# Kernel optimization log

Measured on AMD Instinct MI355X. Metric: run time of the kernel, lower is better.

Reference implementation:

```python
import jax, jax.numpy as jnp
import numpy as np

NUM_EXPERTS = 8
CAPACITY_C = 1.0
ROUTER_TEMP = 1.0
EPS = 1e-10


def reference(x, router_w, router_b, w_gate, b_gate, w_up, b_up, w_down, b_down):
    # x: [B, S, H]
    B, S, H = x.shape
    n_tok = B * S
    k = int(n_tok * CAPACITY_C) // NUM_EXPERTS  # expert capacity (1024 here)

    xf = x.reshape(n_tok, H)  # (b s) h

    # Linear router (dropout p=0 -> identity), computed in float32 as in .float()
    clean_h = xf @ router_w + router_b  # [n_tok, E]

    # Gumbel noise (deterministic key stands in for torch.rand_like)
    u = jax.random.uniform(jax.random.key(42), clean_h.shape, dtype=clean_h.dtype)
    gumbel = -jnp.log(-jnp.log(u + EPS) + EPS)
    h = (clean_h + gumbel) / ROUTER_TEMP

    Sm = jax.nn.softmax(h, axis=-1)  # softmax over experts

    # top-k over the TOKEN dim (dim=0) per expert -> expert-choice routing
    Gt, idxt = jax.lax.top_k(Sm.T, k)  # [E, k]
    G = Gt.T            # [k, E] routing weights
    idx = idxt.T        # [k, E] chosen token indices

    # Gather routed tokens (replaces the one-hot einsum gather exactly:
    # top-k indices are distinct per expert, so one-hot matmul == take)
    toks = jnp.take(xf, idx, axis=0)  # [k, E, H]

    # Shared SwiGLU FFN (group_size=1 -> one expert instance reused E times)
    gate = jax.nn.silu(toks @ w_gate + b_gate)  # [k, E, dff]
    up = toks @ w_up + b_up                      # [k, E, dff]
    e_out = (gate * up) @ w_down + b_down        # [k, E, H]

    # Weight by G and scatter-add back to token positions, summed over experts
    weighted = G[..., None] * e_out              # [k, E, H]
    y = jnp.zeros_like(xf).at[idx.reshape(-1)].add(weighted.reshape(-1, H))
    return y.reshape(B, S, H)


def setup_inputs() -> dict:
    key = jax.random.key(0)
    ks = jax.random.split(key, 6)
    B, S, H, E = 4, 2048, 2048, NUM_EXPERTS
    dff = int(H * 4 * 2 / 3)  # 5461
    sH = 1.0 / np.sqrt(H)
    sF = 1.0 / np.sqrt(dff)
    return {
        "x": jax.random.normal(ks[0], (B, S, H), dtype=jnp.float32),
        "router_w": jax.random.normal(ks[1], (H, E), dtype=jnp.float32) * sH,
        "router_b": jnp.zeros((E,), dtype=jnp.float32),
        "w_gate": jax.random.normal(ks[2], (H, dff), dtype=jnp.float32) * sH,
        "b_gate": jnp.zeros((dff,), dtype=jnp.float32),
        "w_up": jax.random.normal(ks[3], (H, dff), dtype=jnp.float32) * sH,
        "b_up": jnp.zeros((dff,), dtype=jnp.float32),
        "w_down": jax.random.normal(ks[4], (dff, H), dtype=jnp.float32) * sF,
        "b_down": jnp.zeros((H,), dtype=jnp.float32),
    }
```

## Files before the change

### kernel.cpp

```cpp
#include <hip/hip_runtime.h>
#include <cstdint>
#include <cstddef>

#define N_TOK  8192
#define HDIM   2048
#define NEXP   8
#define KCAP   1024
#define DFF    5461
#define DFF_PB 5504
#define ACT_P  5504
#define NT1    (HDIM / 64)
#define NT2    (ACT_P / 64)

typedef unsigned short u16;
typedef short bf16x8 __attribute__((ext_vector_type(8)));
typedef float f32x4  __attribute__((ext_vector_type(4)));

__device__ __forceinline__ u16 f2bf(float f) {
  uint32_t u = __float_as_uint(f);
  uint32_t r = (u + 0x7FFFu + ((u >> 16) & 1u)) >> 16;
  return (u16)r;
}

__device__ __forceinline__ uint32_t rotl32(uint32_t v, int d) {
  return (v << d) | (v >> (32 - d));
}

__device__ uint32_t threefry_bits(uint32_t idx) {
  const uint32_t ks0 = 0u, ks1 = 42u, ks2 = 0u ^ 42u ^ 0x1BD11BDAu;
  uint32_t x0 = 0u + ks0;
  uint32_t x1 = idx + ks1;
#define TFR(d) { x0 += x1; x1 = rotl32(x1, d); x1 ^= x0; }
  TFR(13) TFR(15) TFR(26) TFR(6)
  x0 += ks1; x1 += ks2 + 1u;
  TFR(17) TFR(29) TFR(16) TFR(24)
  x0 += ks2; x1 += ks0 + 2u;
  TFR(13) TFR(15) TFR(26) TFR(6)
  x0 += ks0; x1 += ks1 + 3u;
  TFR(17) TFR(29) TFR(16) TFR(24)
  x0 += ks1; x1 += ks2 + 4u;
  TFR(13) TFR(15) TFR(26) TFR(6)
  x0 += ks2; x1 += ks0 + 5u;
#undef TFR
  return x0 ^ x1;
}

__global__ __launch_bounds__(256) void router_kernel(const float* __restrict__ x,
    const float* __restrict__ rw, const float* __restrict__ rb,
    float* __restrict__ SmT)
{
  const int lane = threadIdx.x & 63;
  const int wid  = threadIdx.x >> 6;
  const int t = blockIdx.x * 4 + wid;
  const float* xr = x + (size_t)t * HDIM;
  float acc[8] = {0.f,0.f,0.f,0.f,0.f,0.f,0.f,0.f};
#pragma unroll
  for (int it = 0; it < HDIM / 64; ++it) {
    int h = lane + it * 64;
    float xv = xr[h];
    const float4* wp = (const float4*)(rw + h * 8);
    float4 w0 = wp[0], w1 = wp[1];
    acc[0] = fmaf(xv, w0.x, acc[0]);
    acc[1] = fmaf(xv, w0.y, acc[1]);
    acc[2] = fmaf(xv, w0.z, acc[2]);
    acc[3] = fmaf(xv, w0.w, acc[3]);
    acc[4] = fmaf(xv, w1.x, acc[4]);
    acc[5] = fmaf(xv, w1.y, acc[5]);
    acc[6] = fmaf(xv, w1.z, acc[6]);
    acc[7] = fmaf(xv, w1.w, acc[7]);
  }
#pragma unroll
  for (int m = 32; m >= 1; m >>= 1) {
#pragma unroll
    for (int e = 0; e < 8; ++e) acc[e] += __shfl_xor(acc[e], m, 64);
  }
  if (lane == 0) {
    float h[8];
#pragma unroll
    for (int e = 0; e < 8; ++e) {
      uint32_t bits = threefry_bits((uint32_t)(t * 8 + e));
      float u = __uint_as_float((bits >> 9) | 0x3f800000u) - 1.0f;
      u = fmaxf(u, 0.0f);
      float g = -logf(-logf(u + 1e-10f) + 1e-10f);
      h[e] = acc[e] + rb[e] + g;
    }
    float mx = h[0];
#pragma unroll
    for (int e = 1; e < 8; ++e) mx = fmaxf(mx, h[e]);
    float ex[8]; float s = 0.f;
#pragma unroll
    for (int e = 0; e < 8; ++e) { ex[e] = expf(h[e] - mx); s += ex[e]; }
#pragma unroll
    for (int e = 0; e < 8; ++e) SmT[e * N_TOK + t] = ex[e] / s;
  }
}

__global__ __launch_bounds__(1024) void select_topk(const float* __restrict__ SmT,
    uint32_t* __restrict__ selTok, float* __restrict__ selW)
{
  const int e = blockIdx.x;
  const int tid = threadIdx.x;
  const float* v = SmT + (size_t)e * N_TOK;
  __shared__ uint32_t hist[256];
  __shared__ uint32_t sh_byte, sh_kk, sh_cnt, sh_eqc;
  uint32_t bitsv[8];
#pragma unroll
  for (int i = 0; i < 8; ++i) bitsv[i] = __float_as_uint(v[tid + i * 1024]);
  uint32_t prefix = 0;
  uint32_t kk = KCAP;
  for (int s = 3; s >= 0; --s) {
    if (tid < 256) hist[tid] = 0;
    __syncthreads();
    uint32_t himask = (s == 3) ? 0u : (0xFFFFFFFFu << ((s + 1) * 8));
#pragma unroll
    for (int i = 0; i < 8; ++i) {
      uint32_t b = bitsv[i];
      if ((b & himask) == prefix) atomicAdd(&hist[(b >> (s * 8)) & 255u], 1u);
    }
    __syncthreads();
    if (tid == 0) {
      uint32_t cum = 0; uint32_t bsel = 0, kn = kk;
      for (int b = 255; b >= 0; --b) {
        uint32_t c = hist[b];
        if (cum + c >= kk) { bsel = (uint32_t)b; kn = kk - cum; break; }
        cum += c;
      }
      sh_byte = bsel; sh_kk = kn;
    }
    __syncthreads();
    prefix |= sh_byte << (s * 8);
    kk = sh_kk;
  }
  const uint32_t T = prefix;
  const uint32_t need = kk;
  if (tid == 0) { sh_cnt = 0; sh_eqc = 0; }
  __syncthreads();
#pragma unroll
  for (int i = 0; i < 8; ++i) {
    uint32_t b = bitsv[i];
    if (b > T) {
      uint32_t p = atomicAdd(&sh_cnt, 1u);
      selTok[e * KCAP + p] = (uint32_t)(tid + i * 1024);
      selW[e * KCAP + p] = __uint_as_float(b);
    } else if (b == T) {
      atomicAdd(&sh_eqc, 1u);
    }
  }
  __syncthreads();
  if (sh_eqc == need) {
#pragma unroll
    for (int i = 0; i < 8; ++i) {
      if (bitsv[i] == T) {
        uint32_t p = atomicAdd(&sh_cnt, 1u);
        selTok[e * KCAP + p] = (uint32_t)(tid + i * 1024);
        selW[e * KCAP + p] = __uint_as_float(T);
      }
    }
  } else if (tid == 0) {
    uint32_t p = sh_cnt, rem = need;
    for (int t = 0; t < N_TOK && rem > 0u; ++t) {
      if (__float_as_uint(v[t]) == T) {
        selTok[e * KCAP + p] = (uint32_t)t;
        selW[e * KCAP + p] = __uint_as_float(T);
        ++p; --rem;
      }
    }
  }
}

__global__ __launch_bounds__(256) void build_inv(const uint32_t* __restrict__ selTok,
    int* __restrict__ inv)
{
  int s = blockIdx.x * 256 + threadIdx.x;
  inv[(s >> 10) * N_TOK + (int)selTok[s]] = s;
}

__global__ __launch_bounds__(256) void gather_kernel(const float* __restrict__ x,
    const uint32_t* __restrict__ selTok, u16* __restrict__ Xsel)
{
  const int slot = blockIdx.x;
  const int tid = threadIdx.x;
  const uint32_t tok = selTok[slot];
  const float4* src = (const float4*)(x + (size_t)tok * HDIM);
  float4 a = src[tid * 2], b = src[tid * 2 + 1];
  union { u16 h[8]; uint4 vv; } pk;
  pk.h[0] = f2bf(a.x); pk.h[1] = f2bf(a.y); pk.h[2] = f2bf(a.z); pk.h[3] = f2bf(a.w);
  pk.h[4] = f2bf(b.x); pk.h[5] = f2bf(b.y); pk.h[6] = f2bf(b.z); pk.h[7] = f2bf(b.w);
  ((uint4*)(Xsel + (size_t)slot * HDIM))[tid] = pk.vv;
}

__global__ __launch_bounds__(256) void transpose_convert(const float* __restrict__ in,
    int rows_in, int cols_in, u16* __restrict__ out, int out_cols)
{
  __shared__ float tile[32][33];
  const int bi = blockIdx.y;
  const int bj = blockIdx.x;
  const int tx = threadIdx.x, ty = threadIdx.y;
#pragma unroll
  for (int t = 0; t < 4; ++t) {
    int r = bi * 32 + ty + t * 8, c = bj * 32 + tx;
    float vv = (r < rows_in && c < cols_in) ? in[(size_t)r * cols_in + c] : 0.0f;
    tile[ty + t * 8][tx] = vv;
  }
  __syncthreads();
#pragma unroll
  for (int t = 0; t < 4; ++t) {
    int oj = bj * 32 + ty + t * 8;
    int oi = bi * 32 + tx;
    out[(size_t)oj * out_cols + oi] = f2bf(tile[tx][ty + t * 8]);
  }
}

#if defined(__has_builtin)
#  if __has_builtin(__builtin_amdgcn_global_load_lds)
#    define HAVE_GLD 1
#  endif
#endif
#ifdef HAVE_GLD
#define STG(gp, lp) __builtin_amdgcn_global_load_lds( \
    (const __attribute__((address_space(1))) void*)(gp), \
    (__attribute__((address_space(3))) void*)(lp), 16, 0, 0)
#define WAITV4() asm volatile("s_waitcnt vmcnt(4)" ::: "memory")
#define WAITV2() asm volatile("s_waitcnt vmcnt(2)" ::: "memory")
#define WAITV0() asm volatile("s_waitcnt vmcnt(0)" ::: "memory")
#else
#define STG(gp, lp) (*(bf16x8*)(lp) = *(const bf16x8*)(gp))
#define WAITV4() asm volatile("s_waitcnt vmcnt(0) lgkmcnt(0)" ::: "memory")
#define WAITV2() asm volatile("s_waitcnt vmcnt(0) lgkmcnt(0)" ::: "memory")
#define WAITV0() asm volatile("s_waitcnt vmcnt(0) lgkmcnt(0)" ::: "memory")
#endif
#define BAR()    __builtin_amdgcn_s_barrier()
#define SCHED0() __builtin_amdgcn_sched_barrier(0)
#define PRIO1()  __builtin_amdgcn_s_setprio(1)
#define PRIO0()  __builtin_amdgcn_s_setprio(0)
#define MFMA(a, b, c) __builtin_amdgcn_mfma_f32_16x16x32_bf16(a, b, c, 0, 0, 0)


__global__ __launch_bounds__(512, 2) void gemm1_kernel(
    const u16* __restrict__ Xsel,
    const u16* __restrict__ WgT,
    const u16* __restrict__ WuT,
    const float* __restrict__ bg, const float* __restrict__ bu,
    u16* __restrict__ act)
{
  __shared__ u16 AL[2][2][8192];
  __shared__ u16 GL[2][8192];
  __shared__ u16 UL[2][8192];

  const int id = blockIdx.x;
  const int wg = (id & 7) * 172 + (id >> 3);
  const int bm = wg & 31;
  const int bn = wg >> 5;

  const int tid = threadIdx.x;
  const int lane = tid & 63, wid = tid >> 6;
  const int wm = wid >> 2, wn = wid & 3;
  const int fr = lane & 15, ck = lane >> 4;
  const int sw0 = (ck ^ (fr & 7)) * 8;
  const int sw1 = sw0 ^ 32;
  const int rA = (wm * 64 + fr) * 64;
  const int rB = (wn * 32 + fr) * 64;

  const int sr = tid >> 3;
  const int sq = (tid & 7) ^ (sr & 7);
  const u16* aS0 = Xsel + (size_t)(bm * 256 + sr) * HDIM + sq * 8;
  const u16* aS1 = aS0 + (size_t)128 * HDIM;
  const u16* gS  = WgT + (size_t)(bn * 128 + sr) * HDIM + sq * 8;
  const u16* uS  = WuT + (size_t)(bn * 128 + sr) * HDIM + sq * 8;

#define ST_A0(kt) { u16* d = &AL[(kt)&1][0][tid*8]; \
    STG(aS0 + (kt)*64, d); STG(aS0 + (kt)*64 + (size_t)64*HDIM, d + 4096); }
#define ST_A1(kt) { u16* d = &AL[(kt)&1][1][tid*8]; \
    STG(aS1 + (kt)*64, d); STG(aS1 + (kt)*64 + (size_t)64*HDIM, d + 4096); }
#define ST_G(kt) { u16* d = &GL[(kt)&1][tid*8]; \
    STG(gS + (kt)*64, d); STG(gS + (kt)*64 + (size_t)64*HDIM, d + 4096); }
#define ST_U(kt) { u16* d = &UL[(kt)&1][tid*8]; \
    STG(uS + (kt)*64, d); STG(uS + (kt)*64 + (size_t)64*HDIM, d + 4096); }

  f32x4 accg[8][2], accu[8][2];
  const f32x4 z4 = {0.f, 0.f, 0.f, 0.f};
#pragma unroll
  for (int i = 0; i < 8; ++i)
#pragma unroll
    for (int n = 0; n < 2; ++n) { accg[i][n] = z4; accu[i][n] = z4; }

  bf16x8 af[4][2], bgf[2][2], buf[2][2];

  ST_A0(0) ST_G(0) ST_U(0) ST_A1(0)
  WAITV4(); BAR();

  for (int kt = 0; kt < NT1; ++kt) {
    const u16* A0 = AL[kt & 1][0];
    const u16* A1 = AL[kt & 1][1];
    const u16* G  = GL[kt & 1];
    const u16* U  = UL[kt & 1];
    const int st = (kt + 1 < NT1);
#pragma unroll
    for (int i = 0; i < 4; ++i) {
      af[i][0] = *(const bf16x8*)&A0[rA + i * 1024 + sw0];
      af[i][1] = *(const bf16x8*)&A0[rA + i * 1024 + sw1];
    }
#pragma unroll
    for (int n = 0; n < 2; ++n) {
      bgf[n][0] = *(const bf16x8*)&G[rB + n * 1024 + sw0];
      bgf[n][1] = *(const bf16x8*)&G[rB + n * 1024 + sw1];
    }
    if (st) ST_A0(kt + 1)
    BAR(); SCHED0();
    PRIO1();
#pragma unroll
    for (int ks = 0; ks < 2; ++ks)
#pragma unroll
      for (int i = 0; i < 4; ++i)
#pragma unroll
        for (int n = 0; n < 2; ++n)
          accg[i][n] = MFMA(af[i][ks], bgf[n][ks], accg[i][n]);
    PRIO0();
    if (st) { WAITV4(); } else { WAITV2(); }
    BAR();
#pragma unroll
    for (int n = 0; n < 2; ++n) {
      buf[n][0] = *(const bf16x8*)&U[rB + n * 1024 + sw0];
      buf[n][1] = *(const bf16x8*)&U[rB + n * 1024 + sw1];
    }
    if (st) ST_G(kt + 1)
    BAR(); SCHED0();
    PRIO1();
#pragma unroll
    for (int ks = 0; ks < 2; ++ks)
#pragma unroll
      for (int i = 0; i < 4; ++i)
#pragma unroll
        for (int n = 0; n < 2; ++n)
          accu[i][n] = MFMA(af[i][ks], buf[n][ks], accu[i][n]);
    PRIO0();
    if (st) { WAITV4(); } else { WAITV0(); }
    BAR();
#pragma unroll
    for (int i = 0; i < 4; ++i) {
      af[i][0] = *(const bf16x8*)&A1[rA + i * 1024 + sw0];
      af[i][1] = *(const bf16x8*)&A1[rA + i * 1024 + sw1];
    }
    if (st) ST_U(kt + 1)
    BAR(); SCHED0();
    PRIO1();
#pragma unroll
    for (int ks = 0; ks < 2; ++ks)
#pragma unroll
      for (int i = 0; i < 4; ++i)
#pragma unroll
        for (int n = 0; n < 2; ++n)
          accg[4 + i][n] = MFMA(af[i][ks], bgf[n][ks], accg[4 + i][n]);
    PRIO0();
    if (st) ST_A1(kt + 1)
    PRIO1();
#pragma unroll
    for (int ks = 0; ks < 2; ++ks)
#pragma unroll
      for (int i = 0; i < 4; ++i)
#pragma unroll
        for (int n = 0; n < 2; ++n)
          accu[4 + i][n] = MFMA(af[i][ks], buf[n][ks], accu[4 + i][n]);
    PRIO0();
    WAITV4();
    BAR();
  }

#pragma unroll
  for (int f = 0; f < 8; ++f) {
    const int rbase = bm * 256 + (f >> 2) * 128 + wm * 64 + (f & 3) * 16 + ck * 4;
#pragma unroll
    for (int v = 0; v < 4; ++v) {
      u16* arow = act + (size_t)(rbase + v) * ACT_P;
#pragma unroll
      for (int n = 0; n < 2; ++n) {
        const int col = bn * 128 + wn * 32 + n * 16 + fr;
        u16 ov = 0;
        if (col < DFF) {
          float gv = accg[f][n][v] + bg[col];
          float uv = accu[f][n][v] + bu[col];
          ov = f2bf((gv / (1.0f + expf(-gv))) * uv);
        }
        arow[col] = ov;
      }
    }
  }
#undef ST_A0
#undef ST_A1
#undef ST_G
#undef ST_U
}

__global__ __launch_bounds__(512, 2) void gemm2_kernel(
    const u16* __restrict__ act,
    const u16* __restrict__ WdT,
    const float* __restrict__ bd,
    const float* __restrict__ selW,
    float* __restrict__ Yslot)
{
  __shared__ u16 AL[2][2][8192];
  __shared__ u16 BL[2][2][8192];

  const int id = blockIdx.x;
  const int wg = (id & 7) * 32 + (id >> 3);
  const int bm = wg & 31, bn = wg >> 5;

  const int tid = threadIdx.x;
  const int lane = tid & 63, wid = tid >> 6;
  const int wm = wid >> 2, wn = wid & 3;
  const int fr = lane & 15, ck = lane >> 4;
  const int sw0 = (ck ^ (fr & 7)) * 8;
  const int sw1 = sw0 ^ 32;
  const int rA = (wm * 64 + fr) * 64;
  const int rB = (wn * 32 + fr) * 64;

  const int sr = tid >> 3;
  const int sq = (tid & 7) ^ (sr & 7);
  const u16* aS0 = act + (size_t)(bm * 256 + sr) * ACT_P + sq * 8;
  const u16* aS1 = aS0 + (size_t)128 * ACT_P;
  const u16* bS0 = WdT + (size_t)(bn * 256 + sr) * ACT_P + sq * 8;
  const u16* bS1 = bS0 + (size_t)128 * ACT_P;

#define ST_A0(kt) { u16* d = &AL[(kt)&1][0][tid*8]; \
    STG(aS0 + (kt)*64, d); STG(aS0 + (kt)*64 + (size_t)64*ACT_P, d + 4096); }
#define ST_A1(kt) { u16* d = &AL[(kt)&1][1][tid*8]; \
    STG(aS1 + (kt)*64, d); STG(aS1 + (kt)*64 + (size_t)64*ACT_P, d + 4096); }
#define ST_B0(kt) { u16* d = &BL[(kt)&1][0][tid*8]; \
    STG(bS0 + (kt)*64, d); STG(bS0 + (kt)*64 + (size_t)64*ACT_P, d + 4096); }
#define ST_B1(kt) { u16* d = &BL[(kt)&1][1][tid*8]; \
    STG(bS1 + (kt)*64, d); STG(bS1 + (kt)*64 + (size_t)64*ACT_P, d + 4096); }

  f32x4 acc[8][4];
  const f32x4 z4 = {0.f, 0.f, 0.f, 0.f};
#pragma unroll
  for (int i = 0; i < 8; ++i)
#pragma unroll
    for (int n = 0; n < 4; ++n) acc[i][n] = z4;

  bf16x8 af[4][2], b0[2][2], b1[2][2];

  ST_A0(0) ST_B0(0) ST_B1(0) ST_A1(0)
  WAITV4(); BAR();

  for (int kt = 0; kt < NT2; ++kt) {
    const u16* A0 = AL[kt & 1][0];
    const u16* A1 = AL[kt & 1][1];
    const u16* B0 = BL[kt & 1][0];
    const u16* B1 = BL[kt & 1][1];
    const int st = (kt + 1 < NT2);
#pragma unroll
    for (int i = 0; i < 4; ++i) {
      af[i][0] = *(const bf16x8*)&A0[rA + i * 1024 + sw0];
      af[i][1] = *(const bf16x8*)&A0[rA + i * 1024 + sw1];
    }
#pragma unroll
    for (int n = 0; n < 2; ++n) {
      b0[n][0] = *(const bf16x8*)&B0[rB + n * 1024 + sw0];
      b0[n][1] = *(const bf16x8*)&B0[rB + n * 1024 + sw1];
    }
    if (st) ST_A0(kt + 1)
    BAR(); SCHED0();
    PRIO1();
#pragma unroll
    for (int ks = 0; ks < 2; ++ks)
#pragma unroll
      for (int i = 0; i < 4; ++i)
#pragma unroll
        for (int n = 0; n < 2; ++n)
          acc[i][n] = MFMA(af[i][ks], b0[n][ks], acc[i][n]);
    PRIO0();
    if (st) { WAITV4(); } else { WAITV2(); }
    BAR();
#pragma unroll
    for (int n = 0; n < 2; ++n) {
      b1[n][0] = *(const bf16x8*)&B1[rB + n * 1024 + sw0];
      b1[n][1] = *(const bf16x8*)&B1[rB + n * 1024 + sw1];
    }
    if (st) ST_B0(kt + 1)
    BAR(); SCHED0();
    PRIO1();
#pragma unroll
    for (int ks = 0; ks < 2; ++ks)
#pragma unroll
      for (int i = 0; i < 4; ++i)
#pragma unroll
        for (int n = 0; n < 2; ++n)
          acc[i][2 + n] = MFMA(af[i][ks], b1[n][ks], acc[i][2 + n]);
    PRIO0();
    if (st) { WAITV4(); } else { WAITV0(); }
    BAR();
#pragma unroll
    for (int i = 0; i < 4; ++i) {
      af[i][0] = *(const bf16x8*)&A1[rA + i * 1024 + sw0];
      af[i][1] = *(const bf16x8*)&A1[rA + i * 1024 + sw1];
    }
    if (st) ST_B1(kt + 1)
    BAR(); SCHED0();
    PRIO1();
#pragma unroll
    for (int ks = 0; ks < 2; ++ks)
#pragma unroll
      for (int i = 0; i < 4; ++i)
#pragma unroll
        for (int n = 0; n < 2; ++n)
          acc[4 + i][n] = MFMA(af[i][ks], b0[n][ks], acc[4 + i][n]);
    PRIO0();
    if (st) ST_A1(kt + 1)
    PRIO1();
#pragma unroll
    for (int ks = 0; ks < 2; ++ks)
#pragma unroll
      for (int i = 0; i < 4; ++i)
#pragma unroll
        for (int n = 0; n < 2; ++n)
          acc[4 + i][2 + n] = MFMA(af[i][ks], b1[n][ks], acc[4 + i][2 + n]);
    PRIO0();
    WAITV4();
    BAR();
  }

#pragma unroll
  for (int f = 0; f < 8; ++f) {
    const int rbase = bm * 256 + (f >> 2) * 128 + wm * 64 + (f & 3) * 16 + ck * 4;
#pragma unroll
    for (int v = 0; v < 4; ++v) {
      const int srow = rbase + v;
      const float w = selW[srow];
      float* yrow = Yslot + (size_t)srow * HDIM;
#pragma unroll
      for (int n = 0; n < 4; ++n) {
        const int col = bn * 256 + (n >> 1) * 128 + wn * 32 + (n & 1) * 16 + fr;
        yrow[col] = w * (acc[f][n][v] + bd[col]);
      }
    }
  }
#undef ST_A0
#undef ST_A1
#undef ST_B0
#undef ST_B1
}

__global__ __launch_bounds__(256) void scatter_kernel(const float* __restrict__ Yslot,
    const int* __restrict__ inv, float* __restrict__ y)
{
  const int t = blockIdx.x;
  const int c = threadIdx.x * 8;
  float4 a0 = {0.f,0.f,0.f,0.f}, a1 = {0.f,0.f,0.f,0.f};
#pragma unroll
  for (int e = 0; e < 8; ++e) {
    const int s = inv[e * N_TOK + t];
    if (s >= 0) {
      const float4* p = (const float4*)(Yslot + (size_t)s * HDIM + c);
      float4 v0 = p[0], v1 = p[1];
      a0.x += v0.x; a0.y += v0.y; a0.z += v0.z; a0.w += v0.w;
      a1.x += v1.x; a1.y += v1.y; a1.z += v1.z; a1.w += v1.w;
    }
  }
  float4* yp = (float4*)(y + (size_t)t * HDIM + c);
  yp[0] = a0; yp[1] = a1;
}

extern "C" void kernel_launch(void* const* d_in, const int* in_sizes, int n_in,
                              void* d_out, int out_size, void* d_ws, size_t ws_size,
                              hipStream_t stream) {
  const float* x      = (const float*)d_in[0];
  const float* rw     = (const float*)d_in[1];
  const float* rb     = (const float*)d_in[2];
  const float* w_gate = (const float*)d_in[3];
  const float* b_gate = (const float*)d_in[4];
  const float* w_up   = (const float*)d_in[5];
  const float* b_up   = (const float*)d_in[6];
  const float* w_down = (const float*)d_in[7];
  const float* b_down = (const float*)d_in[8];
  float* y = (float*)d_out;

  uint8_t* ws = (uint8_t*)d_ws;
  uint32_t* selTok = (uint32_t*)(ws + 0);
  float*    selW   = (float*)(ws + 32768);
  int*      inv    = (int*)(ws + 65536);
  u16*      act    = (u16*)(ws + 327680);
  u16*      Xsel   = (u16*)(ws + 90505216ull);
  u16*      WdT    = (u16*)(ws + 90505216ull);
  float*    Yslot  = (float*)(ws + 113049600ull);
  float*    SmT    = (float*)(ws + 124059648ull);
  u16*      WgT    = (u16*)(ws + 124321792ull);
  u16*      WuT    = (u16*)(ws + 146866176ull);

  hipMemsetAsync(inv, 0xFF, NEXP * N_TOK * sizeof(int), stream);
  transpose_convert<<<dim3(172, 64), dim3(32, 8), 0, stream>>>(w_gate, 2048, DFF, WgT, 2048);
  transpose_convert<<<dim3(172, 64), dim3(32, 8), 0, stream>>>(w_up,   2048, DFF, WuT, 2048);
  router_kernel<<<N_TOK / 4, 256, 0, stream>>>(x, rw, rb, SmT);
  select_topk<<<NEXP, 1024, 0, stream>>>(SmT, selTok, selW);
  build_inv<<<N_TOK / 256, 256, 0, stream>>>(selTok, inv);
  gather_kernel<<<N_TOK, 256, 0, stream>>>(x, selTok, Xsel);
  gemm1_kernel<<<43 * 32, 512, 0, stream>>>(Xsel, WgT, WuT, b_gate, b_up, act);
  transpose_convert<<<dim3(64, 172), dim3(32, 8), 0, stream>>>(w_down, DFF, 2048, WdT, ACT_P);
  gemm2_kernel<<<8 * 32, 512, 0, stream>>>(act, WdT, b_down, selW, Yslot);
  scatter_kernel<<<N_TOK, 256, 0, stream>>>(Yslot, inv, y);
}
```

Before: 911.0 us.

## Trim GEMM pipeline barriers, batch B-tile prefetches, remap gemm1 blocks per XCD

Both GEMM kernels drop the barrier that separated the LDS fragment reads from the next-tile global-to-LDS prefetch. The two B-operand prefetches are now issued together, with a matching vmcnt(6) wait. The second-half gate/up (or b0/b1) MFMA loops are merged into one interleaved loop, and sched barriers now follow the remaining barriers. gemm1 also maps blocks so that each XCD owns four consecutive row tiles, which should improve L2 reuse of the A operand. The SiLU epilogue switches to __expf and a hardware reciprocal. The gains target fewer barrier stalls and longer MFMA runs, at the cost of tighter reliance on correct waitcnt accounting and slightly less precise SiLU.

```diff
diff --git a/kernel.cpp b/kernel.cpp
--- a/kernel.cpp
+++ b/kernel.cpp
@@ -220,11 +220,13 @@
 #define STG(gp, lp) __builtin_amdgcn_global_load_lds( \
     (const __attribute__((address_space(1))) void*)(gp), \
     (__attribute__((address_space(3))) void*)(lp), 16, 0, 0)
+#define WAITV6() asm volatile("s_waitcnt vmcnt(6)" ::: "memory")
 #define WAITV4() asm volatile("s_waitcnt vmcnt(4)" ::: "memory")
 #define WAITV2() asm volatile("s_waitcnt vmcnt(2)" ::: "memory")
 #define WAITV0() asm volatile("s_waitcnt vmcnt(0)" ::: "memory")
 #else
 #define STG(gp, lp) (*(bf16x8*)(lp) = *(const bf16x8*)(gp))
+#define WAITV6() asm volatile("s_waitcnt vmcnt(0) lgkmcnt(0)" ::: "memory")
 #define WAITV4() asm volatile("s_waitcnt vmcnt(0) lgkmcnt(0)" ::: "memory")
 #define WAITV2() asm volatile("s_waitcnt vmcnt(0) lgkmcnt(0)" ::: "memory")
 #define WAITV0() asm volatile("s_waitcnt vmcnt(0) lgkmcnt(0)" ::: "memory")
@@ -248,9 +250,10 @@
   __shared__ u16 UL[2][8192];
 
   const int id = blockIdx.x;
-  const int wg = (id & 7) * 172 + (id >> 3);
-  const int bm = wg & 31;
-  const int bn = wg >> 5;
+  const int xcd = id & 7;
+  const int r = id >> 3;
+  const int bm = xcd * 4 + (r & 3);
+  const int bn = r >> 2;
 
   const int tid = threadIdx.x;
   const int lane = tid & 63, wid = tid >> 6;
@@ -287,7 +290,7 @@
   bf16x8 af[4][2], bgf[2][2], buf[2][2];
 
   ST_A0(0) ST_G(0) ST_U(0) ST_A1(0)
-  WAITV4(); BAR();
+  WAITV4(); BAR(); SCHED0();
 
   for (int kt = 0; kt < NT1; ++kt) {
     const u16* A0 = AL[kt & 1][0];
@@ -306,7 +309,6 @@
       bgf[n][1] = *(const bf16x8*)&G[rB + n * 1024 + sw1];
     }
     if (st) ST_A0(kt + 1)
-    BAR(); SCHED0();
     PRIO1();
 #pragma unroll
     for (int ks = 0; ks < 2; ++ks)
@@ -317,14 +319,13 @@
           accg[i][n] = MFMA(af[i][ks], bgf[n][ks], accg[i][n]);
     PRIO0();
     if (st) { WAITV4(); } else { WAITV2(); }
-    BAR();
+    BAR(); SCHED0();
 #pragma unroll
     for (int n = 0; n < 2; ++n) {
       buf[n][0] = *(const bf16x8*)&U[rB + n * 1024 + sw0];
       buf[n][1] = *(const bf16x8*)&U[rB + n * 1024 + sw1];
     }
-    if (st) ST_G(kt + 1)
-    BAR(); SCHED0();
+    if (st) { ST_G(kt + 1) ST_U(kt + 1) }
     PRIO1();
 #pragma unroll
     for (int ks = 0; ks < 2; ++ks)
@@ -334,24 +335,13 @@
         for (int n = 0; n < 2; ++n)
           accu[i][n] = MFMA(af[i][ks], buf[n][ks], accu[i][n]);
     PRIO0();
-    if (st) { WAITV4(); } else { WAITV0(); }
-    BAR();
+    if (st) { WAITV6(); } else { WAITV0(); }
+    BAR(); SCHED0();
 #pragma unroll
     for (int i = 0; i < 4; ++i) {
       af[i][0] = *(const bf16x8*)&A1[rA + i * 1024 + sw0];
       af[i][1] = *(const bf16x8*)&A1[rA + i * 1024 + sw1];
     }
-    if (st) ST_U(kt + 1)
-    BAR(); SCHED0();
-    PRIO1();
-#pragma unroll
-    for (int ks = 0; ks < 2; ++ks)
-#pragma unroll
-      for (int i = 0; i < 4; ++i)
-#pragma unroll
-        for (int n = 0; n < 2; ++n)
-          accg[4 + i][n] = MFMA(af[i][ks], bgf[n][ks], accg[4 + i][n]);
-    PRIO0();
     if (st) ST_A1(kt + 1)
     PRIO1();
 #pragma unroll
@@ -359,11 +349,13 @@
 #pragma unroll
       for (int i = 0; i < 4; ++i)
 #pragma unroll
-        for (int n = 0; n < 2; ++n)
+        for (int n = 0; n < 2; ++n) {
+          accg[4 + i][n] = MFMA(af[i][ks], bgf[n][ks], accg[4 + i][n]);
           accu[4 + i][n] = MFMA(af[i][ks], buf[n][ks], accu[4 + i][n]);
+        }
     PRIO0();
     WAITV4();
-    BAR();
+    BAR(); SCHED0();
   }
 
 #pragma unroll
@@ -379,7 +371,9 @@
         if (col < DFF) {
           float gv = accg[f][n][v] + bg[col];
           float uv = accu[f][n][v] + bu[col];
-          ov = f2bf((gv / (1.0f + expf(-gv))) * uv);
+          float e = __expf(-gv);
+          float sv = gv * __builtin_amdgcn_rcpf(1.0f + e);
+          ov = f2bf(sv * uv);
         }
         arow[col] = ov;
       }
@@ -440,7 +434,7 @@
   bf16x8 af[4][2], b0[2][2], b1[2][2];
 
   ST_A0(0) ST_B0(0) ST_B1(0) ST_A1(0)
-  WAITV4(); BAR();
+  WAITV4(); BAR(); SCHED0();
 
   for (int kt = 0; kt < NT2; ++kt) {
     const u16* A0 = AL[kt & 1][0];
@@ -459,7 +453,6 @@
       b0[n][1] = *(const bf16x8*)&B0[rB + n * 1024 + sw1];
     }
     if (st) ST_A0(kt + 1)
-    BAR(); SCHED0();
     PRIO1();
 #pragma unroll
     for (int ks = 0; ks < 2; ++ks)
@@ -470,14 +463,13 @@
           acc[i][n] = MFMA(af[i][ks], b0[n][ks], acc[i][n]);
     PRIO0();
     if (st) { WAITV4(); } else { WAITV2(); }
-    BAR();
+    BAR(); SCHED0();
 #pragma unroll
     for (int n = 0; n < 2; ++n) {
       b1[n][0] = *(const bf16x8*)&B1[rB + n * 1024 + sw0];
       b1[n][1] = *(const bf16x8*)&B1[rB + n * 1024 + sw1];
     }
-    if (st) ST_B0(kt + 1)
-    BAR(); SCHED0();
+    if (st) { ST_B0(kt + 1) ST_B1(kt + 1) }
     PRIO1();
 #pragma unroll
     for (int ks = 0; ks < 2; ++ks)
@@ -487,24 +479,13 @@
         for (int n = 0; n < 2; ++n)
           acc[i][2 + n] = MFMA(af[i][ks], b1[n][ks], acc[i][2 + n]);
     PRIO0();
-    if (st) { WAITV4(); } else { WAITV0(); }
-    BAR();
+    if (st) { WAITV6(); } else { WAITV0(); }
+    BAR(); SCHED0();
 #pragma unroll
     for (int i = 0; i < 4; ++i) {
       af[i][0] = *(const bf16x8*)&A1[rA + i * 1024 + sw0];
       af[i][1] = *(const bf16x8*)&A1[rA + i * 1024 + sw1];
     }
-    if (st) ST_B1(kt + 1)
-    BAR(); SCHED0();
-    PRIO1();
-#pragma unroll
-    for (int ks = 0; ks < 2; ++ks)
-#pragma unroll
-      for (int i = 0; i < 4; ++i)
-#pragma unroll
-        for (int n = 0; n < 2; ++n)
-          acc[4 + i][n] = MFMA(af[i][ks], b0[n][ks], acc[4 + i][n]);
-    PRIO0();
     if (st) ST_A1(kt + 1)
     PRIO1();
 #pragma unroll
@@ -512,11 +493,13 @@
 #pragma unroll
       for (int i = 0; i < 4; ++i)
 #pragma unroll
-        for (int n = 0; n < 2; ++n)
+        for (int n = 0; n < 2; ++n) {
+          acc[4 + i][n]     = MFMA(af[i][ks], b0[n][ks], acc[4 + i][n]);
           acc[4 + i][2 + n] = MFMA(af[i][ks], b1[n][ks], acc[4 + i][2 + n]);
+        }
     PRIO0();
     WAITV4();
-    BAR();
+    BAR(); SCHED0();
   }
 
 #pragma unroll
```

New measurement: 874.7 us. -4.0%, faster.
